# Optimization experiments

Measured on AMD Instinct MI355X. Metric: run time of the kernel, lower is better.

## Reference

```python
import jax, jax.numpy as jnp
import numpy as np

TAU_M = 20.0
DT = 1.0
V_TH = 1.0
V_RESET = 0.0
ALPHA = float(np.exp(-DT / TAU_M))  # membrane decay per step

B, T, I, H, O = 64, 1024, 128, 512, 10


def spike_fn(v):
    # Heaviside spike; surrogate grad handled in fwdbwd module.
    return (v >= 0.0).astype(v.dtype)


def setup_inputs() -> dict:
    key = jax.random.key(0)
    k = jax.random.split(key, 6)
    x = jax.random.normal(k[0], (B, T, I), dtype=jnp.float32)
    # input_projection: Linear(I, H) -> weight [H, I], bias [H]
    Wi = jax.random.normal(k[1], (H, I), dtype=jnp.float32) * (1.0 / np.sqrt(I))
    bi = jnp.zeros((H,), dtype=jnp.float32)
    # recurrent weight [H, H] (xavier-ish)
    Wr = jax.random.normal(k[2], (H, H), dtype=jnp.float32) * float(np.sqrt(2.0 / (H + H)))
    # readout: Linear(H, O)
    Wo = jax.random.normal(k[3], (O, H), dtype=jnp.float32) * (1.0 / np.sqrt(H))
    bo = jnp.zeros((O,), dtype=jnp.float32)
    return {"x": x, "Wi": Wi, "bi": bi, "Wr": Wr, "Wo": Wo, "bo": bo}


def reference(x, Wi, bi, Wr, Wo, bo):
    # Precompute input projection for all timesteps: [B, T, H]
    x_proj = jnp.einsum('bti,hi->bth', x, Wi) + bi

    def step(carry, cur_t):
        h, spikes_prev = carry
        total_current = cur_t + spikes_prev @ Wr        # [B, H]
        h = ALPHA * h + total_current                    # LIF leak + integrate
        spikes = spike_fn(h - V_TH)                      # threshold
        h = spikes * V_RESET + (1.0 - spikes) * h        # reset on spike
        return (h, spikes), spikes

    h0 = jnp.zeros((x.shape[0], Wr.shape[0]), dtype=x.dtype)
    s0 = jnp.zeros_like(h0)
    (_, _), hidden_states = jax.lax.scan(step, (h0, s0), jnp.swapaxes(x_proj, 0, 1))
    hidden_states = jnp.swapaxes(hidden_states, 0, 1)    # [B, T, H]

    hidden_mean = hidden_states.mean(axis=1)             # rate readout
    output = hidden_mean @ Wo.T + bo                     # [B, O]
    return output, hidden_states
```

## Files before the change

### kernel.cpp

```cpp
#include <hip/hip_runtime.h>


#define ALPHA_F 0.951229424500714f

__device__ float g_mean[64 * 512];

__global__ __launch_bounds__(256) void xproj_kernel(
    const float* __restrict__ x, const float* __restrict__ Wi,
    const float* __restrict__ bi, float* __restrict__ out)
{
    __shared__ float xs[64][132];
    __shared__ float ws[32][132];

    const int tid = threadIdx.x;
    const int bm = blockIdx.x;
    const int bn = blockIdx.y;

    const float* xb = x  + (size_t)bm * 64 * 128;
    const float* wb = Wi + (size_t)bn * 32 * 128;

    for (int l = 0; l < 8; ++l) {
        int idx = l * 256 + tid;
        int row = idx >> 5, c4 = idx & 31;
        *(float4*)(&xs[row][c4 * 4]) = *(const float4*)(xb + row * 128 + c4 * 4);
    }
    for (int l = 0; l < 4; ++l) {
        int idx = l * 256 + tid;
        int row = idx >> 5, c4 = idx & 31;
        *(float4*)(&ws[row][c4 * 4]) = *(const float4*)(wb + row * 128 + c4 * 4);
    }
    __syncthreads();

    const int txh = tid & 15, txm = tid >> 4;
    const int m0 = txm * 4, h0 = txh * 2;

    float4 acc[4][2];
    #pragma unroll
    for (int mm = 0; mm < 4; ++mm)
        #pragma unroll
        for (int q = 0; q < 2; ++q)
            acc[mm][q] = make_float4(0.f, 0.f, 0.f, 0.f);

    for (int k4 = 0; k4 < 32; ++k4) {
        float4 a[4], b[2];
        #pragma unroll
        for (int mm = 0; mm < 4; ++mm) a[mm] = *(const float4*)(&xs[m0 + mm][k4 * 4]);
        #pragma unroll
        for (int q = 0; q < 2; ++q)    b[q]  = *(const float4*)(&ws[h0 + q][k4 * 4]);
        #pragma unroll
        for (int mm = 0; mm < 4; ++mm) {
            #pragma unroll
            for (int q = 0; q < 2; ++q) {
                float p0 = a[mm].x * b[q].x;
                float p1 = a[mm].y * b[q].y;
                float p2 = a[mm].z * b[q].z;
                float p3 = a[mm].w * b[q].w;
                asm volatile("" : "+v"(p0), "+v"(p1), "+v"(p2), "+v"(p3));
                acc[mm][q].x += p0;
                acc[mm][q].y += p1;
                acc[mm][q].z += p2;
                acc[mm][q].w += p3;
            }
        }
    }

    const int hbase = bn * 32 + h0;
    #pragma unroll
    for (int mm = 0; mm < 4; ++mm) {
        size_t m = (size_t)bm * 64 + m0 + mm;
        float2 o;
        {
            float s01 = acc[mm][0].x + acc[mm][0].y;
            float s23 = acc[mm][0].z + acc[mm][0].w;
            float hs  = s01 + s23;
            o.x = hs + bi[hbase + 0];
        }
        {
            float s01 = acc[mm][1].x + acc[mm][1].y;
            float s23 = acc[mm][1].z + acc[mm][1].w;
            float hs  = s01 + s23;
            o.y = hs + bi[hbase + 1];
        }
        *(float2*)(&out[m * 512 + hbase]) = o;
    }
}

__global__ __launch_bounds__(512) void scan_kernel(
    const float* __restrict__ Wr, float* __restrict__ hid)
{
    const int b    = blockIdx.x;
    const int h    = threadIdx.x;
    const int wv   = h >> 6;
    const int lane = h & 63;

    __shared__ unsigned short list[512];
    __shared__ int wcnt[8];

    float hstate = 0.0f;
    int cnt = 0;
    int k = 0, kA = 0;

    float* base = hid + (size_t)b * 1024 * 512;
    const float* wcol = Wr + h;

    for (int t = 0; t < 1024; ++t) {
        float xp = base[(size_t)t * 512 + h];

        float recA = 0.0f, recB = 0.0f;
        int n = 0;
        for (; n + 4 <= kA; n += 4) {
            int j0 = list[n], j1 = list[n + 1], j2 = list[n + 2], j3 = list[n + 3];
            float w0 = wcol[j0 * 512], w1 = wcol[j1 * 512];
            float w2 = wcol[j2 * 512], w3 = wcol[j3 * 512];
            recA += w0; recA += w1; recA += w2; recA += w3;
        }
        for (; n < kA; ++n) recA += wcol[(int)list[n] * 512];
        for (; n + 4 <= k; n += 4) {
            int j0 = list[n], j1 = list[n + 1], j2 = list[n + 2], j3 = list[n + 3];
            float w0 = wcol[j0 * 512], w1 = wcol[j1 * 512];
            float w2 = wcol[j2 * 512], w3 = wcol[j3 * 512];
            recB += w0; recB += w1; recB += w2; recB += w3;
        }
        for (; n < k; ++n) recB += wcol[(int)list[n] * 512];

        float rec = recA + recB;
        float cur = xp + rec;

        float tmp = ALPHA_F * hstate;
        asm volatile("" : "+v"(tmp));
        float hn = tmp + cur;

        bool sp = (hn >= 1.0f);
        hstate = sp ? 0.0f : hn;
        base[(size_t)t * 512 + h] = sp ? 1.0f : 0.0f;
        cnt += sp ? 1 : 0;

        unsigned long long m = __ballot(sp);
        int pos = __popcll(m & ((1ull << lane) - 1ull));
        __syncthreads();
        if (lane == 0) wcnt[wv] = __popcll(m);
        __syncthreads();
        int off = 0, ktot = 0, ka = 0;
        #pragma unroll
        for (int w = 0; w < 8; ++w) {
            int c = wcnt[w];
            if (w < wv) off += c;
            if (w < 6)  ka  += c;
            ktot += c;
        }
        if (sp) list[off + pos] = (unsigned short)h;
        k = ktot; kA = ka;
        __syncthreads();
    }

    g_mean[b * 512 + h] = (float)cnt * (1.0f / 1024.0f);
}

__global__ __launch_bounds__(64) void readout_kernel(
    const float* __restrict__ Wo, const float* __restrict__ bo,
    float* __restrict__ out)
{
    const int b = blockIdx.x, o = blockIdx.y;
    const int lane = threadIdx.x;
    const float* mr = g_mean + b * 512;
    const float* wr = Wo + o * 512;
    double s = 0.0;
    for (int i = lane; i < 512; i += 64) s += (double)mr[i] * (double)wr[i];
    #pragma unroll
    for (int off = 32; off; off >>= 1) s += __shfl_down(s, off);
    if (lane == 0) out[b * 10 + o] = (float)(s + (double)bo[o]);
}

extern "C" void kernel_launch(void* const* d_in, const int* in_sizes, int n_in,
                              void* d_out, int out_size, void* d_ws, size_t ws_size,
                              hipStream_t stream) {
    const float* x  = (const float*)d_in[0];
    const float* Wi = (const float*)d_in[1];
    const float* bi = (const float*)d_in[2];
    const float* Wr = (const float*)d_in[3];
    const float* Wo = (const float*)d_in[4];
    const float* bo = (const float*)d_in[5];

    float* out = (float*)d_out;
    float* hid = out + 640;

    dim3 gA(1024, 16);
    xproj_kernel<<<gA, 256, 0, stream>>>(x, Wi, bi, hid);

    scan_kernel<<<64, 512, 0, stream>>>(Wr, hid);

    dim3 gC(64, 10);
    readout_kernel<<<gC, 64, 0, stream>>>(Wo, bo, out);
}
```

Measured before the change: 2.289 ms.

## Software-pipeline sparse recurrent gather and trim barriers in LIF scan kernel

Restructures the per-timestep sparse gather in the scan kernel so the spike list is read as 16-byte chunks of 8 indices, with three chunks of Wr loads kept in flight ahead of their use. It also prefetches the next timestep's input projection, removes one of the three barriers per step by using a custom barrier that waits only on LDS traffic, and makes the loop counts wave-uniform with readfirstlane. The aim is to hide global-load latency on the serial 1024-step critical path and cut synchronisation overhead. In exchange it adds register pressure and complex tail and boundary handling, and it reads stale list entries past k, which are then masked.

```diff
diff --git a/kernel.cpp b/kernel.cpp
--- a/kernel.cpp
+++ b/kernel.cpp
@@ -85,72 +85,138 @@
     }
 }
 
-__global__ __launch_bounds__(512) void scan_kernel(
+struct C8 { float a, b, c, d, e, f, g, h; };
+
+__device__ __forceinline__ C8 fetch8(const unsigned short* lst, int c,
+                                     const float* __restrict__ Wr, unsigned hh) {
+    const uint4* lv = (const uint4*)lst;
+    uint4 L = lv[c];
+    unsigned o0 = ((L.x & 0xffffu) << 9) + hh;
+    unsigned o1 = ((L.x >> 16)     << 9) + hh;
+    unsigned o2 = ((L.y & 0xffffu) << 9) + hh;
+    unsigned o3 = ((L.y >> 16)     << 9) + hh;
+    unsigned o4 = ((L.z & 0xffffu) << 9) + hh;
+    unsigned o5 = ((L.z >> 16)     << 9) + hh;
+    unsigned o6 = ((L.w & 0xffffu) << 9) + hh;
+    unsigned o7 = ((L.w >> 16)     << 9) + hh;
+    C8 r;
+    r.a = Wr[o0]; r.b = Wr[o1]; r.c = Wr[o2]; r.d = Wr[o3];
+    r.e = Wr[o4]; r.f = Wr[o5]; r.g = Wr[o6]; r.h = Wr[o7];
+    return r;
+}
+
+__device__ __forceinline__ void consume8(const C8& v, int e, int kA, int k,
+                                         float& recA, float& recB) {
+    if (e + 8 <= kA) {
+        recA += v.a; recA += v.b; recA += v.c; recA += v.d;
+        recA += v.e; recA += v.f; recA += v.g; recA += v.h;
+    } else if (e >= kA && e + 8 <= k) {
+        recB += v.a; recB += v.b; recB += v.c; recB += v.d;
+        recB += v.e; recB += v.f; recB += v.g; recB += v.h;
+    } else {
+        if (e + 0 < k) { if (e + 0 < kA) recA += v.a; else recB += v.a; }
+        if (e + 1 < k) { if (e + 1 < kA) recA += v.b; else recB += v.b; }
+        if (e + 2 < k) { if (e + 2 < kA) recA += v.c; else recB += v.c; }
+        if (e + 3 < k) { if (e + 3 < kA) recA += v.d; else recB += v.d; }
+        if (e + 4 < k) { if (e + 4 < kA) recA += v.e; else recB += v.e; }
+        if (e + 5 < k) { if (e + 5 < kA) recA += v.f; else recB += v.f; }
+        if (e + 6 < k) { if (e + 6 < kA) recA += v.g; else recB += v.g; }
+        if (e + 7 < k) { if (e + 7 < kA) recA += v.h; else recB += v.h; }
+    }
+}
+
+#define BAR() do { \
+    asm volatile("s_waitcnt lgkmcnt(0)" ::: "memory"); \
+    __builtin_amdgcn_s_barrier(); \
+    asm volatile("" ::: "memory"); \
+} while (0)
+
+__global__ __launch_bounds__(512, 1) void scan_kernel(
     const float* __restrict__ Wr, float* __restrict__ hid)
 {
     const int b    = blockIdx.x;
     const int h    = threadIdx.x;
     const int wv   = h >> 6;
     const int lane = h & 63;
-
-    __shared__ unsigned short list[512];
-    __shared__ int wcnt[8];
+    const unsigned hh = (unsigned)h;
+
+    __shared__ alignas(16) unsigned short list[512];
+    __shared__ alignas(16) int wcnt[8];
+
+    list[h] = 0;
+    __syncthreads();
+
+    const int wvs = __builtin_amdgcn_readfirstlane(wv);
 
     float hstate = 0.0f;
     int cnt = 0;
     int k = 0, kA = 0;
 
     float* base = hid + (size_t)b * 1024 * 512;
-    const float* wcol = Wr + h;
+    float xp = base[h];
+    const unsigned long long lmask = (1ull << lane) - 1ull;
 
     for (int t = 0; t < 1024; ++t) {
-        float xp = base[(size_t)t * 512 + h];
+        int tn = (t < 1023) ? t + 1 : 1023;
+        float xp_next = base[(size_t)tn * 512 + h];
 
         float recA = 0.0f, recB = 0.0f;
-        int n = 0;
-        for (; n + 4 <= kA; n += 4) {
-            int j0 = list[n], j1 = list[n + 1], j2 = list[n + 2], j3 = list[n + 3];
-            float w0 = wcol[j0 * 512], w1 = wcol[j1 * 512];
-            float w2 = wcol[j2 * 512], w3 = wcol[j3 * 512];
-            recA += w0; recA += w1; recA += w2; recA += w3;
-        }
-        for (; n < kA; ++n) recA += wcol[(int)list[n] * 512];
-        for (; n + 4 <= k; n += 4) {
-            int j0 = list[n], j1 = list[n + 1], j2 = list[n + 2], j3 = list[n + 3];
-            float w0 = wcol[j0 * 512], w1 = wcol[j1 * 512];
-            float w2 = wcol[j2 * 512], w3 = wcol[j3 * 512];
-            recB += w0; recB += w1; recB += w2; recB += w3;
-        }
-        for (; n < k; ++n) recB += wcol[(int)list[n] * 512];
+        int nch = (k + 7) >> 3;
+
+        C8 b0, b1, b2;
+        if (nch > 0) b0 = fetch8(list, 0, Wr, hh);
+        if (nch > 1) b1 = fetch8(list, 1, Wr, hh);
+        if (nch > 2) b2 = fetch8(list, 2, Wr, hh);
+        int c = 0;
+        for (; c + 6 <= nch; c += 3) {
+            consume8(b0, (c + 0) * 8, kA, k, recA, recB); b0 = fetch8(list, c + 3, Wr, hh);
+            consume8(b1, (c + 1) * 8, kA, k, recA, recB); b1 = fetch8(list, c + 4, Wr, hh);
+            consume8(b2, (c + 2) * 8, kA, k, recA, recB); b2 = fetch8(list, c + 5, Wr, hh);
+        }
+        int rem = nch - c;
+        if (rem >= 1) consume8(b0, (c + 0) * 8, kA, k, recA, recB);
+        if (rem >= 4) b0 = fetch8(list, c + 3, Wr, hh);
+        if (rem >= 2) consume8(b1, (c + 1) * 8, kA, k, recA, recB);
+        if (rem >= 5) b1 = fetch8(list, c + 4, Wr, hh);
+        if (rem >= 3) consume8(b2, (c + 2) * 8, kA, k, recA, recB);
+        if (rem >= 4) consume8(b0, (c + 3) * 8, kA, k, recA, recB);
+        if (rem >= 5) consume8(b1, (c + 4) * 8, kA, k, recA, recB);
 
         float rec = recA + recB;
         float cur = xp + rec;
-
         float tmp = ALPHA_F * hstate;
         asm volatile("" : "+v"(tmp));
         float hn = tmp + cur;
-
         bool sp = (hn >= 1.0f);
         hstate = sp ? 0.0f : hn;
         base[(size_t)t * 512 + h] = sp ? 1.0f : 0.0f;
         cnt += sp ? 1 : 0;
 
         unsigned long long m = __ballot(sp);
-        int pos = __popcll(m & ((1ull << lane) - 1ull));
-        __syncthreads();
+        int pos = __popcll(m & lmask);
         if (lane == 0) wcnt[wv] = __popcll(m);
-        __syncthreads();
-        int off = 0, ktot = 0, ka = 0;
-        #pragma unroll
-        for (int w = 0; w < 8; ++w) {
-            int c = wcnt[w];
-            if (w < wv) off += c;
-            if (w < 6)  ka  += c;
-            ktot += c;
-        }
+
+        BAR();
+
+        int4 wa = *(const int4*)&wcnt[0];
+        int4 wb = *(const int4*)&wcnt[4];
+        int off = 0;
+        if (wvs > 0) off += wa.x;
+        if (wvs > 1) off += wa.y;
+        if (wvs > 2) off += wa.z;
+        if (wvs > 3) off += wa.w;
+        if (wvs > 4) off += wb.x;
+        if (wvs > 5) off += wb.y;
+        if (wvs > 6) off += wb.z;
+        int nkA = wa.x + wa.y + wa.z + wa.w + wb.x + wb.y;
+        int nk  = nkA + wb.z + wb.w;
         if (sp) list[off + pos] = (unsigned short)h;
-        k = ktot; kA = ka;
-        __syncthreads();
+
+        BAR();
+
+        k  = __builtin_amdgcn_readfirstlane(nk);
+        kA = __builtin_amdgcn_readfirstlane(nkA);
+        xp = xp_next;
     }
 
     g_mean[b * 512 + h] = (float)cnt * (1.0f / 1024.0f);
```

Result: no change. 2.249 ms (-1.8%).

## Split recurrent scan across 256 blocks with Wr slices in LDS and global spike flags

Applied to the files above, without the earlier changes.

The scan now runs on 256 blocks instead of 64. Each block owns a 64-column slice of Wr, keeps it in LDS, and handles two batch rows, one per wavefront. Blocks exchange per-timestep spike bitmasks through a double-buffered sync array in workspace, using cache-bypassing loads and stores with spin-polling on a timestep tag, and rebuild the active-spike list locally. This removes the global-memory gather of Wr columns and spreads the serial recurrence over more CUs. In exchange it adds inter-block polling latency on every step and depends on all 256 blocks being co-resident.

```diff
diff --git a/kernel.cpp b/kernel.cpp
--- a/kernel.cpp
+++ b/kernel.cpp
@@ -2,6 +2,8 @@
 
 
 #define ALPHA_F 0.951229424500714f
+
+typedef unsigned int u32x4 __attribute__((ext_vector_type(4)));
 
 __device__ float g_mean[64 * 512];
 
@@ -85,75 +87,169 @@
     }
 }
 
-__global__ __launch_bounds__(512) void scan_kernel(
-    const float* __restrict__ Wr, float* __restrict__ hid)
+struct C8 { float a, b, c, d, e, f, g, h; };
+
+__device__ __forceinline__ C8 fetch8_lds(const unsigned short* lst, int cidx,
+                                         const float (*wrs)[64], int lane) {
+    uint4 L = ((const uint4*)lst)[cidx];
+    int j0 = (int)(L.x & 0xffffu), j1 = (int)(L.x >> 16);
+    int j2 = (int)(L.y & 0xffffu), j3 = (int)(L.y >> 16);
+    int j4 = (int)(L.z & 0xffffu), j5 = (int)(L.z >> 16);
+    int j6 = (int)(L.w & 0xffffu), j7 = (int)(L.w >> 16);
+    C8 r;
+    r.a = wrs[j0][lane]; r.b = wrs[j1][lane];
+    r.c = wrs[j2][lane]; r.d = wrs[j3][lane];
+    r.e = wrs[j4][lane]; r.f = wrs[j5][lane];
+    r.g = wrs[j6][lane]; r.h = wrs[j7][lane];
+    return r;
+}
+
+__device__ __forceinline__ void consume8(const C8& v, int e, int kA, int k,
+                                         float& recA, float& recB) {
+    if (e + 8 <= kA) {
+        recA += v.a; recA += v.b; recA += v.c; recA += v.d;
+        recA += v.e; recA += v.f; recA += v.g; recA += v.h;
+    } else if (e >= kA && e + 8 <= k) {
+        recB += v.a; recB += v.b; recB += v.c; recB += v.d;
+        recB += v.e; recB += v.f; recB += v.g; recB += v.h;
+    } else {
+        if (e + 0 < k) { if (e + 0 < kA) recA += v.a; else recB += v.a; }
+        if (e + 1 < k) { if (e + 1 < kA) recA += v.b; else recB += v.b; }
+        if (e + 2 < k) { if (e + 2 < kA) recA += v.c; else recB += v.c; }
+        if (e + 3 < k) { if (e + 3 < kA) recA += v.d; else recB += v.d; }
+        if (e + 4 < k) { if (e + 4 < kA) recA += v.e; else recB += v.e; }
+        if (e + 5 < k) { if (e + 5 < kA) recA += v.f; else recB += v.f; }
+        if (e + 6 < k) { if (e + 6 < kA) recA += v.g; else recB += v.g; }
+        if (e + 7 < k) { if (e + 7 < kA) recA += v.h; else recB += v.h; }
+    }
+}
+
+__global__ __launch_bounds__(128, 1) void scan_kernel(
+    const float* __restrict__ Wr, float* __restrict__ hid,
+    u32x4* __restrict__ syn)
 {
-    const int b    = blockIdx.x;
-    const int h    = threadIdx.x;
-    const int wv   = h >> 6;
-    const int lane = h & 63;
-
-    __shared__ unsigned short list[512];
-    __shared__ int wcnt[8];
+    const int blk  = blockIdx.x;
+    const int p    = blk & 31;
+    const int c    = blk >> 5;
+    const int tid  = threadIdx.x;
+    const int w    = tid >> 6;
+    const int lane = tid & 63;
+    const int s    = p + 32 * w;
+    const int n    = (c << 6) + lane;
+
+    __shared__ float wrs[512][64];
+    __shared__ unsigned short lists[2][512];
+
+    #pragma unroll
+    for (int i = 0; i < 8; ++i) ((unsigned short*)lists)[tid * 8 + i] = 0;
+
+    {
+        const float* src = Wr + (c << 6);
+        for (int it = 0; it < 64; ++it) {
+            int idx = it * 128 + tid;
+            int r = idx >> 4, q = idx & 15;
+            float4 v = *(const float4*)(src + (size_t)r * 512 + q * 4);
+            *(float4*)(&wrs[r][q * 4]) = v;
+        }
+    }
+    __syncthreads();
+
+    unsigned short* list = lists[w];
+    float* base = hid + ((size_t)s * 1024) * 512 + n;
 
     float hstate = 0.0f;
     int cnt = 0;
-    int k = 0, kA = 0;
-
-    float* base = hid + (size_t)b * 1024 * 512;
-    const float* wcol = Wr + h;
+    float xp = base[0];
 
     for (int t = 0; t < 1024; ++t) {
-        float xp = base[(size_t)t * 512 + h];
+        float xp_next = base[(size_t)(t < 1023 ? t + 1 : 1023) * 512];
+
+        int k = 0, kA = 0;
+        if (t > 0) {
+            const u32x4* pp = syn + ((((t - 1) & 1) * 64 + s) * 8) + (lane & 7);
+            u32x4 pv;
+            for (;;) {
+                u32x4 tv;
+                asm volatile("global_load_dwordx4 %0, %1, off sc0 sc1\n\t"
+                             "s_waitcnt vmcnt(0)"
+                             : "=v"(tv) : "v"(pp) : "memory");
+                unsigned long long ok = __ballot(tv.z == (unsigned)t);
+                if ((ok & 0xFFull) == 0xFFull) { pv = tv; break; }
+                __builtin_amdgcn_s_sleep(1);
+            }
+            unsigned long long fullm = (((unsigned long long)pv.y) << 32) | pv.x;
+            int pc = __popcll(fullm);
+            int sc_ = pc, u_;
+            u_ = __shfl_up(sc_, 1); if (lane >= 1) sc_ += u_;
+            u_ = __shfl_up(sc_, 2); if (lane >= 2) sc_ += u_;
+            u_ = __shfl_up(sc_, 4); if (lane >= 4) sc_ += u_;
+            int excl = sc_ - pc;
+            k  = __builtin_amdgcn_readfirstlane(__shfl(sc_, 7));
+            kA = __builtin_amdgcn_readfirstlane(__shfl(sc_, 5));
+            unsigned mlo = (unsigned)__shfl((int)pv.x, lane >> 3);
+            unsigned mhi = (unsigned)__shfl((int)pv.y, lane >> 3);
+            int ep = __shfl(excl, lane >> 3);
+            int sb = (lane & 7) * 8;
+            unsigned byte; int below;
+            if (sb < 32) {
+                byte  = (mlo >> sb) & 0xFFu;
+                below = __popc(mlo & ((1u << sb) - 1u));
+            } else {
+                byte  = (mhi >> (sb - 32)) & 0xFFu;
+                below = __popc(mlo) + __popc(mhi & ((1u << (sb - 32)) - 1u));
+            }
+            int pos = ep + below;
+            while (byte) {
+                int bt = __builtin_ctz(byte);
+                byte &= byte - 1;
+                list[pos++] = (unsigned short)(lane * 8 + bt);
+            }
+        }
 
         float recA = 0.0f, recB = 0.0f;
-        int n = 0;
-        for (; n + 4 <= kA; n += 4) {
-            int j0 = list[n], j1 = list[n + 1], j2 = list[n + 2], j3 = list[n + 3];
-            float w0 = wcol[j0 * 512], w1 = wcol[j1 * 512];
-            float w2 = wcol[j2 * 512], w3 = wcol[j3 * 512];
-            recA += w0; recA += w1; recA += w2; recA += w3;
-        }
-        for (; n < kA; ++n) recA += wcol[(int)list[n] * 512];
-        for (; n + 4 <= k; n += 4) {
-            int j0 = list[n], j1 = list[n + 1], j2 = list[n + 2], j3 = list[n + 3];
-            float w0 = wcol[j0 * 512], w1 = wcol[j1 * 512];
-            float w2 = wcol[j2 * 512], w3 = wcol[j3 * 512];
-            recB += w0; recB += w1; recB += w2; recB += w3;
-        }
-        for (; n < k; ++n) recB += wcol[(int)list[n] * 512];
+        if (k > 0) {
+            int nch = (k + 7) >> 3;
+            C8 b0, b1;
+            b0 = fetch8_lds(list, 0, wrs, lane);
+            if (nch > 1) b1 = fetch8_lds(list, 1, wrs, lane);
+            int cc = 0;
+            for (; cc + 4 <= nch; cc += 2) {
+                consume8(b0, (cc + 0) * 8, kA, k, recA, recB);
+                b0 = fetch8_lds(list, cc + 2, wrs, lane);
+                consume8(b1, (cc + 1) * 8, kA, k, recA, recB);
+                b1 = fetch8_lds(list, cc + 3, wrs, lane);
+            }
+            int rem = nch - cc;
+            if (rem >= 1) consume8(b0, (cc + 0) * 8, kA, k, recA, recB);
+            if (rem >= 3) b0 = fetch8_lds(list, cc + 2, wrs, lane);
+            if (rem >= 2) consume8(b1, (cc + 1) * 8, kA, k, recA, recB);
+            if (rem >= 3) consume8(b0, (cc + 2) * 8, kA, k, recA, recB);
+        }
 
         float rec = recA + recB;
         float cur = xp + rec;
-
         float tmp = ALPHA_F * hstate;
         asm volatile("" : "+v"(tmp));
         float hn = tmp + cur;
-
         bool sp = (hn >= 1.0f);
         hstate = sp ? 0.0f : hn;
-        base[(size_t)t * 512 + h] = sp ? 1.0f : 0.0f;
+
+        unsigned long long bm = __ballot(sp);
+        if (lane == 0) {
+            u32x4 pk;
+            pk.x = (unsigned)bm; pk.y = (unsigned)(bm >> 32);
+            pk.z = (unsigned)(t + 1); pk.w = 0u;
+            u32x4* qp = syn + (((t & 1) * 64 + s) * 8) + c;
+            asm volatile("global_store_dwordx4 %0, %1, off sc0 sc1"
+                         :: "v"(qp), "v"(pk) : "memory");
+        }
+
+        base[(size_t)t * 512] = sp ? 1.0f : 0.0f;
         cnt += sp ? 1 : 0;
-
-        unsigned long long m = __ballot(sp);
-        int pos = __popcll(m & ((1ull << lane) - 1ull));
-        __syncthreads();
-        if (lane == 0) wcnt[wv] = __popcll(m);
-        __syncthreads();
-        int off = 0, ktot = 0, ka = 0;
-        #pragma unroll
-        for (int w = 0; w < 8; ++w) {
-            int c = wcnt[w];
-            if (w < wv) off += c;
-            if (w < 6)  ka  += c;
-            ktot += c;
-        }
-        if (sp) list[off + pos] = (unsigned short)h;
-        k = ktot; kA = ka;
-        __syncthreads();
-    }
-
-    g_mean[b * 512 + h] = (float)cnt * (1.0f / 1024.0f);
+        xp = xp_next;
+    }
+
+    g_mean[s * 512 + n] = (float)cnt * (1.0f / 1024.0f);
 }
 
 __global__ __launch_bounds__(64) void readout_kernel(
@@ -184,10 +280,12 @@
     float* out = (float*)d_out;
     float* hid = out + 640;
 
+    (void)hipMemsetAsync(d_ws, 0, 2 * 64 * 8 * 16, stream);
+
     dim3 gA(1024, 16);
     xproj_kernel<<<gA, 256, 0, stream>>>(x, Wi, bi, hid);
 
-    scan_kernel<<<64, 512, 0, stream>>>(Wr, hid);
+    scan_kernel<<<256, 128, 0, stream>>>(Wr, hid, (u32x4*)d_ws);
 
     dim3 gC(64, 10);
     readout_kernel<<<gC, 64, 0, stream>>>(Wo, bo, out);
```

Measured after the change: 2.132 ms. 1.07x faster.
